# Kernel optimization log

Hardware: AMD Instinct MI355X
Metric: run time of the kernel (lower is better)

The kernel has to match this reference:

```python
import jax, jax.numpy as jnp
import numpy as np

D_MODEL, D_HIDDEN, N_EXPERTS = 1024, 4096, 8
CAP_FACTOR, LBL_COEF, ZLOSS_COEF = 1.25, 0.01, 0.0


def setup_inputs() -> dict:
    key = jax.random.key(0)
    ks = jax.random.split(key, 4)
    B, T = 4, 2048
    x = jax.random.normal(ks[0], (B, T, D_MODEL), dtype=jnp.float32)
    # router linear
    Wr = jax.random.normal(ks[1], (D_MODEL, N_EXPERTS), jnp.float32) / np.sqrt(D_MODEL).astype(np.float32)
    br = jnp.zeros((N_EXPERTS,), jnp.float32)
    # per-expert MLP: fc1 [D->H], gelu, fc2 [H->D]
    W1 = jax.random.normal(ks[2], (N_EXPERTS, D_MODEL, D_HIDDEN), jnp.float32) / np.sqrt(D_MODEL).astype(np.float32)
    b1 = jnp.zeros((N_EXPERTS, D_HIDDEN), jnp.float32)
    W2 = jax.random.normal(ks[3], (N_EXPERTS, D_HIDDEN, D_MODEL), jnp.float32) / np.sqrt(D_HIDDEN).astype(np.float32)
    b2 = jnp.zeros((N_EXPERTS, D_MODEL), jnp.float32)
    return {"x": x, "Wr": Wr, "br": br, "W1": W1, "b1": b1, "W2": W2, "b2": b2}


def reference(x, Wr, br, W1, b1, W2, b2):
    B, T, D = x.shape
    N = B * T
    E = Wr.shape[1]
    cap = int(CAP_FACTOR * (N / E) + 1)  # static Python int

    h = x.reshape(N, D)
    # --- Top1Router ---
    logits = h @ Wr + br                              # [N, E]
    probs = jax.nn.softmax(logits, axis=-1)
    top1 = jnp.argmax(probs, axis=-1)                 # [N]
    w = jnp.take_along_axis(probs, top1[:, None], axis=1)  # [N, 1]
    assign = jax.nn.one_hot(top1, E, dtype=jnp.float32)    # constant wrt grads
    importance = probs.mean(axis=0)
    load = jax.lax.stop_gradient(assign).mean(axis=0)
    lb_loss = E * jnp.sum(importance * load)
    z_loss = jnp.mean(jax.nn.logsumexp(logits, axis=-1) ** 2)

    # --- capacity-based dispatch (first `cap` tokens per expert, token order) ---
    pos = (jnp.cumsum(assign, axis=0) * assign).sum(axis=-1).astype(jnp.int32) - 1  # [N] slot within expert
    keep = pos < cap
    slot = jnp.where(keep, pos, cap)  # dropped tokens -> overflow slot `cap`
    xe = jnp.zeros((E, cap + 1, D), x.dtype).at[top1, slot].set(h)[:, :cap]  # [E, cap, D]

    # --- per-expert MLP as grouped GEMMs ---
    he = jax.nn.gelu(jnp.einsum('ecd,edh->ech', xe, W1) + b1[:, None, :])    # [E, cap, H]
    ye = jnp.einsum('ech,ehd->ecd', he, W2) + b2[:, None, :]                 # [E, cap, D]

    # --- combine (gather back, scale by router weight, zero dropped) ---
    out = ye[top1, jnp.minimum(pos, cap - 1)] * w   # [N, D]
    out = jnp.where(keep[:, None], out, jnp.zeros((), x.dtype))
    y = out.reshape(B, T, D)
    aux = LBL_COEF * lb_loss + ZLOSS_COEF * z_loss
    return (y, aux)
```

## Files before the change

### kernel.cpp

```cpp
#include <hip/hip_runtime.h>
#include <hip/hip_bf16.h>

#define N_TOK 8192
#define DM    1024
#define DH    4096
#define NE    8
#define CAP   1281
#define CAPR  1408
#define ISTR  1536

typedef unsigned short u16;
typedef __attribute__((ext_vector_type(8))) __bf16 bf16x8;
typedef __attribute__((ext_vector_type(8))) short short8;
typedef __attribute__((ext_vector_type(4))) float f4;

__device__ __forceinline__ u16 f2bf(float f){
  union { float f; unsigned u; } v; v.f = f;
  unsigned r = v.u + 0x7fffu + ((v.u >> 16) & 1u);
  return (u16)(r >> 16);
}

__device__ __forceinline__ float gelu_fast(float v){
  float u = 0.7978845608028654f * (v + 0.044715f * v * v * v);
  return v * __builtin_amdgcn_rcpf(1.0f + __expf(-2.0f * u));
}

__device__ __forceinline__ void gl2lds16(const void* g, void* l){
  __builtin_amdgcn_global_load_lds((const __attribute__((address_space(1))) void*)g,
                                   (__attribute__((address_space(3))) void*)l, 16, 0, 0);
}

__global__ __launch_bounds__(256) void cvt_x_k(const float* __restrict__ in, u16* __restrict__ out){
  int i = blockIdx.x * 256 + threadIdx.x;
  const f4* p = (const f4*)in + (size_t)i * 2;
  f4 a = p[0], b = p[1];
  short8 o;
  o[0]=(short)f2bf(a[0]); o[1]=(short)f2bf(a[1]); o[2]=(short)f2bf(a[2]); o[3]=(short)f2bf(a[3]);
  o[4]=(short)f2bf(b[0]); o[5]=(short)f2bf(b[1]); o[6]=(short)f2bf(b[2]); o[7]=(short)f2bf(b[3]);
  *(short8*)(out + (size_t)i*8) = o;
}

__global__ __launch_bounds__(256) void tcvt_k(const float* __restrict__ in, u16* __restrict__ out,
                                              int K, int Nn){
  __shared__ float tile[64][68];
  size_t mb = (size_t)blockIdx.z * (size_t)K * (size_t)Nn;
  const float* ip = in + mb;
  u16* op = out + mb;
  int n0 = blockIdx.x*64, k0 = blockIdx.y*64;
  int t = threadIdx.x;
  int kr = t>>4, nc = (t&15)*4;
  #pragma unroll
  for (int ii=0;ii<4;ii++){
    f4 v = *(const f4*)&ip[(size_t)(k0+kr+16*ii)*Nn + n0 + nc];
    tile[kr+16*ii][nc+0] = v[0]; tile[kr+16*ii][nc+1] = v[1];
    tile[kr+16*ii][nc+2] = v[2]; tile[kr+16*ii][nc+3] = v[3];
  }
  __syncthreads();
  int nr = t>>2, kc = (t&3)*16;
  short8 o0, o1;
  #pragma unroll
  for (int c=0;c<8;c++){
    o0[c] = (short)f2bf(tile[kc+c][nr]);
    o1[c] = (short)f2bf(tile[kc+8+c][nr]);
  }
  *(short8*)&op[(size_t)(n0+nr)*K + k0 + kc] = o0;
  *(short8*)&op[(size_t)(n0+nr)*K + k0 + kc + 8] = o1;
}

__global__ __launch_bounds__(256) void router_k(const float* __restrict__ x, const float* __restrict__ Wr,
    const float* __restrict__ br, int* __restrict__ top1, float* __restrict__ wgt,
    float* __restrict__ impSum){
  __shared__ float pSh[4][8];
  int wid = threadIdx.x >> 6, lane = threadIdx.x & 63;
  int n = blockIdx.x * 4 + wid;
  const float* xr = x + (size_t)n * DM;
  float acc[8];
  #pragma unroll
  for (int e=0;e<8;e++) acc[e]=0.f;
  #pragma unroll
  for (int c=0;c<4;c++){
    int d0 = c*256 + lane*4;
    f4 xv = *(const f4*)(xr + d0);
    #pragma unroll
    for (int j=0;j<4;j++){
      const float* wrow = Wr + (size_t)(d0+j)*NE;
      float xs = xv[j];
      #pragma unroll
      for (int e=0;e<8;e++) acc[e] = fmaf(xs, wrow[e], acc[e]);
    }
  }
  #pragma unroll
  for (int off=32; off>0; off>>=1){
    #pragma unroll
    for (int e=0;e<8;e++) acc[e] += __shfl_down(acc[e], off, 64);
  }
  if (lane==0){
    float lg[8]; float mx = -1e30f;
    #pragma unroll
    for (int e=0;e<8;e++){ lg[e] = acc[e] + br[e]; mx = fmaxf(mx, lg[e]); }
    float p[8], s=0.f;
    #pragma unroll
    for (int e=0;e<8;e++){ p[e] = expf(lg[e]-mx); s += p[e]; }
    int bt=0; float bv=lg[0];
    #pragma unroll
    for (int e=1;e<8;e++){ if (lg[e]>bv){ bv=lg[e]; bt=e; } }
    float inv = 1.f/s;
    top1[n] = bt; wgt[n] = p[bt]*inv;
    #pragma unroll
    for (int e=0;e<8;e++) pSh[wid][e] = p[e]*inv;
  }
  __syncthreads();
  if (threadIdx.x < 8){
    int e = threadIdx.x;
    atomicAdd(&impSum[e], pSh[0][e]+pSh[1][e]+pSh[2][e]+pSh[3][e]);
  }
}

__global__ __launch_bounds__(1024) void scan_k(const int* __restrict__ top1, int* __restrict__ idx,
    int* __restrict__ cnt, int* __restrict__ rawcnt, int* __restrict__ dropList,
    int* __restrict__ nDrop, const float* __restrict__ impSum, float* __restrict__ auxOut){
  __shared__ int waveCnt[16][8];
  __shared__ int wavePre[16][8];
  __shared__ int chunkTot[8];
  __shared__ int base_s[8];
  int tid = threadIdx.x, wid = tid>>6, lane = tid&63;
  if (tid < 8) base_s[tid] = 0;
  __syncthreads();
  for (int c=0;c<8;c++){
    int t = c*1024 + tid;
    int e = top1[t];
    int myPre = 0;
    #pragma unroll
    for (int ex=0; ex<8; ex++){
      unsigned long long mk = __ballot(e == ex);
      if (lane == 0) waveCnt[wid][ex] = __popcll(mk);
      if (ex == e) myPre = __popcll(mk & ((1ull<<lane)-1ull));
    }
    __syncthreads();
    if (tid < 8){
      int run = 0;
      for (int wv=0; wv<16; wv++){ wavePre[wv][tid] = run; run += waveCnt[wv][tid]; }
      chunkTot[tid] = run;
    }
    __syncthreads();
    int pos = base_s[e] + wavePre[wid][e] + myPre;
    if (pos < CAP) idx[e*ISTR + pos] = t;
    else { int d = atomicAdd(nDrop, 1); dropList[d] = t; }
    __syncthreads();
    if (tid < 8) base_s[tid] += chunkTot[tid];
    __syncthreads();
  }
  if (tid < 8){
    rawcnt[tid] = base_s[tid];
    cnt[tid] = base_s[tid] < CAP ? base_s[tid] : CAP;
  }
  if (tid == 0){
    float s = 0.f;
    for (int e=0;e<8;e++) s += (impSum[e]*(1.f/N_TOK)) * ((float)base_s[e]*(1.f/N_TOK));
    *auxOut = 0.01f * 8.f * s;
  }
}

__global__ __launch_bounds__(256) void zdrop_k(const int* __restrict__ dropList,
    const int* __restrict__ nDrop, float* __restrict__ y){
  int nd = *nDrop;
  for (int i = blockIdx.x; i < nd; i += gridDim.x){
    int t = dropList[i];
    f4* row = (f4*)(y + (size_t)t * DM);
    f4 z; z[0]=0.f; z[1]=0.f; z[2]=0.f; z[3]=0.f;
    row[threadIdx.x] = z;
  }
}

#define SA(buf, h, kt) do{ \
  gl2lds16(aS[(h)*2+0] + (size_t)(kt)*64, &lds[(buf)*16384 + ((h)*2+0)*4096 + t*8]); \
  gl2lds16(aS[(h)*2+1] + (size_t)(kt)*64, &lds[(buf)*16384 + ((h)*2+1)*4096 + t*8]); }while(0)
#define SBg(buf, h, kt) do{ \
  gl2lds16(bS[(h)*2+0] + (size_t)(kt)*64, &lds[32768 + (buf)*16384 + ((h)*2+0)*4096 + t*8]); \
  gl2lds16(bS[(h)*2+1] + (size_t)(kt)*64, &lds[32768 + (buf)*16384 + ((h)*2+1)*4096 + t*8]); }while(0)

#define LDA(buf, m, kk) (*(const bf16x8*)&lds[(buf)*16384 + (aBase ^ ((kk)*32)) + (m)*1024])
#define LDB(buf, n, kk) (*(const bf16x8*)&lds[32768 + (buf)*16384 + (bBase ^ ((kk)*32)) + (n)*1024])

#define PHASE(buf, q, STAGES, PREBAR) do{ \
  bf16x8 a_[2][2]; \
  if ((q)==0){ \
    _Pragma("unroll") for (int n_=0;n_<4;n_++) \
      _Pragma("unroll") for (int kk_=0;kk_<2;kk_++) Bf[n_][kk_] = LDB(buf, n_, kk_); \
  } \
  _Pragma("unroll") for (int j_=0;j_<2;j_++) \
    _Pragma("unroll") for (int kk_=0;kk_<2;kk_++) a_[j_][kk_] = LDA(buf, 2*(q)+j_, kk_); \
  STAGES; \
  __builtin_amdgcn_s_barrier(); \
  asm volatile("s_waitcnt lgkmcnt(0)" ::: "memory"); \
  __builtin_amdgcn_sched_barrier(0); \
  __builtin_amdgcn_s_setprio(1); \
  _Pragma("unroll") for (int j_=0;j_<2;j_++) \
    _Pragma("unroll") for (int n_=0;n_<4;n_++) \
      _Pragma("unroll") for (int kk_=0;kk_<2;kk_++) \
        acc[2*(q)+j_][n_] = __builtin_amdgcn_mfma_f32_16x16x32_bf16(a_[j_][kk_], Bf[n_][kk_], acc[2*(q)+j_][n_], 0,0,0); \
  __builtin_amdgcn_s_setprio(0); \
  PREBAR; \
  __builtin_amdgcn_s_barrier(); \
}while(0)

#define VMC4 asm volatile("s_waitcnt vmcnt(4)" ::: "memory")
#define NOP2 (void)0

__global__ __launch_bounds__(512, 2) void gemm1_k(
    const u16* __restrict__ Xb, const u16* __restrict__ W1T,
    const float* __restrict__ b1, const int* __restrict__ idx,
    const int* __restrict__ cnt, u16* __restrict__ He)
{
  int e = blockIdx.z, mt = blockIdx.y, nt = blockIdx.x;
  int cn = cnt[e];
  if (mt*256 >= cn) return;
  __shared__ __align__(16) u16 lds[65536];
  int t = threadIdx.x, lane = t&63, wid = t>>6;
  int waveM = wid>>2, waveN = wid&3;
  int rA = lane&15, kb = lane>>4, s = rA&7;

  const u16* aS[4]; const u16* bS[4];
  #pragma unroll
  for (int j=0;j<4;j++){
    int pos = j*512 + t;
    int row = pos>>3, ch = pos&7;
    int gcb = ch ^ (row&7);
    int slotrow = mt*256 + row;
    int token = (slotrow < cn) ? idx[e*ISTR + slotrow] : 0;
    aS[j] = Xb + (size_t)token*DM + gcb*8;
    bS[j] = W1T + ((size_t)e*DH + nt*256 + row)*DM + gcb*8;
  }
  f4 acc[8][4];
  #pragma unroll
  for (int m=0;m<8;m++)
    #pragma unroll
    for (int n=0;n<4;n++)
      #pragma unroll
      for (int j=0;j<4;j++) acc[m][n][j]=0.f;

  int aBase = (waveM*128 + rA)*64 + (kb ^ s)*8;
  int bBase = (waveN*64  + rA)*64 + (kb ^ s)*8;
  bf16x8 Bf[4][2];

  SBg(0,0,0); SBg(0,1,0); SA(0,0,0); SA(0,1,0); SBg(1,0,1); SBg(1,1,1);
  VMC4;
  __builtin_amdgcn_s_barrier();

  const int NT = DM/64;
  #pragma unroll 1
  for (int i=0;i<NT/2;i++){
    int kt1 = 2*i+1;
    int kt2 = (2*i+2 < NT) ? 2*i+2 : NT-1;
    int kt3 = (2*i+3 < NT) ? 2*i+3 : NT-1;
    PHASE(0,0, SA(1,0,kt1), NOP2);
    PHASE(0,1, { SA(1,1,kt1); SBg(0,0,kt2); }, NOP2);
    PHASE(0,2, SBg(0,1,kt2), NOP2);
    PHASE(0,3, NOP2, VMC4);
    PHASE(1,0, SA(0,0,kt2), NOP2);
    PHASE(1,1, { SA(0,1,kt2); SBg(1,0,kt3); }, NOP2);
    PHASE(1,2, SBg(1,1,kt3), NOP2);
    PHASE(1,3, NOP2, VMC4);
  }
  asm volatile("s_waitcnt vmcnt(0)" ::: "memory");

  int rG = lane>>4;
  #pragma unroll
  for (int n=0;n<4;n++){
    int col = nt*256 + waveN*64 + n*16 + rA;
    float bias = b1[e*DH + col];
    #pragma unroll
    for (int m=0;m<8;m++){
      int slot = mt*256 + waveM*128 + m*16 + rG*4;
      if (slot < CAPR){
        u16* dst = He + ((size_t)e*CAPR + slot)*DH + col;
        #pragma unroll
        for (int j=0;j<4;j++){
          float v = acc[m][n][j] + bias;
          dst[(size_t)j*DH] = f2bf(gelu_fast(v));
        }
      }
    }
  }
}

__global__ __launch_bounds__(512, 2) void gemm2_k(
    const u16* __restrict__ He, const u16* __restrict__ W2T,
    const float* __restrict__ b2, const int* __restrict__ idx,
    const int* __restrict__ cnt, const float* __restrict__ wgt,
    float* __restrict__ y)
{
  int e = blockIdx.z, mt = blockIdx.y, nt = blockIdx.x;
  int cn = cnt[e];
  if (mt*256 >= cn) return;
  __shared__ __align__(16) u16 lds[65536];
  int t = threadIdx.x, lane = t&63, wid = t>>6;
  int waveM = wid>>2, waveN = wid&3;
  int rA = lane&15, kb = lane>>4, s = rA&7;

  const u16* aS[4]; const u16* bS[4];
  #pragma unroll
  for (int j=0;j<4;j++){
    int pos = j*512 + t;
    int row = pos>>3, ch = pos&7;
    int gcb = ch ^ (row&7);
    int srow = mt*256 + row; if (srow >= cn) srow = cn-1;
    aS[j] = He  + ((size_t)e*CAPR + srow)*DH + gcb*8;
    bS[j] = W2T + ((size_t)e*DM + nt*256 + row)*DH + gcb*8;
  }
  f4 acc[8][4];
  #pragma unroll
  for (int m=0;m<8;m++)
    #pragma unroll
    for (int n=0;n<4;n++)
      #pragma unroll
      for (int j=0;j<4;j++) acc[m][n][j]=0.f;

  int aBase = (waveM*128 + rA)*64 + (kb ^ s)*8;
  int bBase = (waveN*64  + rA)*64 + (kb ^ s)*8;
  bf16x8 Bf[4][2];

  SBg(0,0,0); SBg(0,1,0); SA(0,0,0); SA(0,1,0); SBg(1,0,1); SBg(1,1,1);
  VMC4;
  __builtin_amdgcn_s_barrier();

  const int NT = DH/64;
  #pragma unroll 1
  for (int i=0;i<NT/2;i++){
    int kt1 = 2*i+1;
    int kt2 = (2*i+2 < NT) ? 2*i+2 : NT-1;
    int kt3 = (2*i+3 < NT) ? 2*i+3 : NT-1;
    PHASE(0,0, SA(1,0,kt1), NOP2);
    PHASE(0,1, { SA(1,1,kt1); SBg(0,0,kt2); }, NOP2);
    PHASE(0,2, SBg(0,1,kt2), NOP2);
    PHASE(0,3, NOP2, VMC4);
    PHASE(1,0, SA(0,0,kt2), NOP2);
    PHASE(1,1, { SA(0,1,kt2); SBg(1,0,kt3); }, NOP2);
    PHASE(1,2, SBg(1,1,kt3), NOP2);
    PHASE(1,3, NOP2, VMC4);
  }
  asm volatile("s_waitcnt vmcnt(0)" ::: "memory");

  int rG = lane>>4;
  float bias_[4];
  #pragma unroll
  for (int n=0;n<4;n++) bias_[n] = b2[e*DM + nt*256 + waveN*64 + n*16 + rA];
  #pragma unroll
  for (int m=0;m<8;m++){
    int slot0 = mt*256 + waveM*128 + m*16 + rG*4;
    #pragma unroll
    for (int j=0;j<4;j++){
      int slot = slot0 + j;
      bool valid = slot < cn;
      int tk = valid ? idx[e*ISTR + slot] : 0;
      float wv = valid ? wgt[tk] : 0.f;
      float* yr = y + (size_t)tk*DM;
      #pragma unroll
      for (int n=0;n<4;n++){
        int col = nt*256 + waveN*64 + n*16 + rA;
        if (valid) yr[col] = (acc[m][n][j] + bias_[n]) * wv;
      }
    }
  }
}

extern "C" void kernel_launch(void* const* d_in, const int* in_sizes, int n_in,
                              void* d_out, int out_size, void* d_ws, size_t ws_size,
                              hipStream_t stream){
  const float* x  = (const float*)d_in[0];
  const float* Wr = (const float*)d_in[1];
  const float* br = (const float*)d_in[2];
  const float* W1 = (const float*)d_in[3];
  const float* b1 = (const float*)d_in[4];
  const float* W2 = (const float*)d_in[5];
  const float* b2 = (const float*)d_in[6];
  float* y = (float*)d_out;

  char* ws = (char*)d_ws;
  u16* Xb  = (u16*)(ws);
  u16* W1T = (u16*)(ws + 16777216ull);
  u16* W2T = (u16*)(ws + 16777216ull + 67108864ull);
  u16* He  = (u16*)(ws + 16777216ull + 2ull*67108864ull);
  char* tail = ws + 16777216ull + 2ull*67108864ull + (size_t)NE*CAPR*DH*2ull;
  int*   top1 = (int*)(tail);
  float* wgt  = (float*)(tail + 32768);
  int*   idx  = (int*)(tail + 65536);
  int*   drop = (int*)(tail + 65536 + 49152);
  float* impSum = (float*)(tail + 65536 + 49152 + 32768);
  int*   nDrop  = (int*)((char*)impSum + 32);
  int*   cnt    = nDrop + 1;
  int*   rawcnt = cnt + 8;

  hipMemsetAsync(impSum, 0, 64, stream);

  cvt_x_k<<<4096, 256, 0, stream>>>(x, Xb);
  tcvt_k<<<dim3(64,16,8), 256, 0, stream>>>(W1, W1T, DM, DH);
  tcvt_k<<<dim3(16,64,8), 256, 0, stream>>>(W2, W2T, DH, DM);
  router_k<<<2048, 256, 0, stream>>>(x, Wr, br, top1, wgt, impSum);
  scan_k<<<1, 1024, 0, stream>>>(top1, idx, cnt, rawcnt, drop, nDrop, impSum,
                                 y + (size_t)N_TOK*DM);
  zdrop_k<<<64, 256, 0, stream>>>(drop, nDrop, y);
  gemm1_k<<<dim3(DH/256, 6, NE), 512, 0, stream>>>(Xb, W1T, b1, idx, cnt, He);
  gemm2_k<<<dim3(DM/256, 6, NE), 512, 0, stream>>>(He, W2T, b2, idx, cnt, wgt, y);

  (void)in_sizes; (void)n_in; (void)out_size; (void)ws_size;
}
```

Baseline: 376.1 us.

## Fuse x bf16 conversion into router and restructure GEMM k-tile pipeline

The standalone x-to-bf16 conversion kernel is removed, and the router now writes the bf16 copy while it already reads x. This saves one launch and one full pass over x. Both expert GEMMs also replace the eight-phase double-buffer schedule with a per-k-tile macro that waits on vmcnt(6) and issues A and B prefetches for the next tiles between the four MFMA sub-phases. The new schedule changes load ordering and barrier placement, so it risks races or less overlap if the wait counts are wrong.

```diff
diff --git a/kernel.cpp b/kernel.cpp
--- a/kernel.cpp
+++ b/kernel.cpp
@@ -12,6 +12,7 @@
 typedef unsigned short u16;
 typedef __attribute__((ext_vector_type(8))) __bf16 bf16x8;
 typedef __attribute__((ext_vector_type(8))) short short8;
+typedef __attribute__((ext_vector_type(4))) short s16x4;
 typedef __attribute__((ext_vector_type(4))) float f4;
 
 __device__ __forceinline__ u16 f2bf(float f){
@@ -28,16 +29,6 @@
 __device__ __forceinline__ void gl2lds16(const void* g, void* l){
   __builtin_amdgcn_global_load_lds((const __attribute__((address_space(1))) void*)g,
                                    (__attribute__((address_space(3))) void*)l, 16, 0, 0);
-}
-
-__global__ __launch_bounds__(256) void cvt_x_k(const float* __restrict__ in, u16* __restrict__ out){
-  int i = blockIdx.x * 256 + threadIdx.x;
-  const f4* p = (const f4*)in + (size_t)i * 2;
-  f4 a = p[0], b = p[1];
-  short8 o;
-  o[0]=(short)f2bf(a[0]); o[1]=(short)f2bf(a[1]); o[2]=(short)f2bf(a[2]); o[3]=(short)f2bf(a[3]);
-  o[4]=(short)f2bf(b[0]); o[5]=(short)f2bf(b[1]); o[6]=(short)f2bf(b[2]); o[7]=(short)f2bf(b[3]);
-  *(short8*)(out + (size_t)i*8) = o;
 }
 
 __global__ __launch_bounds__(256) void tcvt_k(const float* __restrict__ in, u16* __restrict__ out,
@@ -68,12 +59,13 @@
 }
 
 __global__ __launch_bounds__(256) void router_k(const float* __restrict__ x, const float* __restrict__ Wr,
-    const float* __restrict__ br, int* __restrict__ top1, float* __restrict__ wgt,
-    float* __restrict__ impSum){
+    const float* __restrict__ br, u16* __restrict__ Xb, int* __restrict__ top1,
+    float* __restrict__ wgt, float* __restrict__ impSum){
   __shared__ float pSh[4][8];
   int wid = threadIdx.x >> 6, lane = threadIdx.x & 63;
   int n = blockIdx.x * 4 + wid;
   const float* xr = x + (size_t)n * DM;
+  u16* xbr = Xb + (size_t)n * DM;
   float acc[8];
   #pragma unroll
   for (int e=0;e<8;e++) acc[e]=0.f;
@@ -81,6 +73,10 @@
   for (int c=0;c<4;c++){
     int d0 = c*256 + lane*4;
     f4 xv = *(const f4*)(xr + d0);
+    s16x4 xb;
+    #pragma unroll
+    for (int j=0;j<4;j++) xb[j] = (short)f2bf(xv[j]);
+    *(s16x4*)(xbr + d0) = xb;
     #pragma unroll
     for (int j=0;j<4;j++){
       const float* wrow = Wr + (size_t)(d0+j)*NE;
@@ -172,40 +168,63 @@
   }
 }
 
-#define SA(buf, h, kt) do{ \
-  gl2lds16(aS[(h)*2+0] + (size_t)(kt)*64, &lds[(buf)*16384 + ((h)*2+0)*4096 + t*8]); \
-  gl2lds16(aS[(h)*2+1] + (size_t)(kt)*64, &lds[(buf)*16384 + ((h)*2+1)*4096 + t*8]); }while(0)
-#define SBg(buf, h, kt) do{ \
-  gl2lds16(bS[(h)*2+0] + (size_t)(kt)*64, &lds[32768 + (buf)*16384 + ((h)*2+0)*4096 + t*8]); \
-  gl2lds16(bS[(h)*2+1] + (size_t)(kt)*64, &lds[32768 + (buf)*16384 + ((h)*2+1)*4096 + t*8]); }while(0)
 
 #define LDA(buf, m, kk) (*(const bf16x8*)&lds[(buf)*16384 + (aBase ^ ((kk)*32)) + (m)*1024])
 #define LDB(buf, n, kk) (*(const bf16x8*)&lds[32768 + (buf)*16384 + (bBase ^ ((kk)*32)) + (n)*1024])
 
-#define PHASE(buf, q, STAGES, PREBAR) do{ \
-  bf16x8 a_[2][2]; \
-  if ((q)==0){ \
-    _Pragma("unroll") for (int n_=0;n_<4;n_++) \
-      _Pragma("unroll") for (int kk_=0;kk_<2;kk_++) Bf[n_][kk_] = LDB(buf, n_, kk_); \
-  } \
-  _Pragma("unroll") for (int j_=0;j_<2;j_++) \
-    _Pragma("unroll") for (int kk_=0;kk_<2;kk_++) a_[j_][kk_] = LDA(buf, 2*(q)+j_, kk_); \
-  STAGES; \
-  __builtin_amdgcn_s_barrier(); \
-  asm volatile("s_waitcnt lgkmcnt(0)" ::: "memory"); \
-  __builtin_amdgcn_sched_barrier(0); \
-  __builtin_amdgcn_s_setprio(1); \
+#define SA_J(buf, j, kc) gl2lds16(aS[j] + (size_t)(kc)*64, &lds[(buf)*16384 + ((j)*512 + t)*8])
+#define SB_ALLM(buf, kc) do{ \
+  gl2lds16(bS[0] + (size_t)(kc)*64, &lds[32768 + (buf)*16384 + (0*512 + t)*8]); \
+  gl2lds16(bS[1] + (size_t)(kc)*64, &lds[32768 + (buf)*16384 + (1*512 + t)*8]); \
+  gl2lds16(bS[2] + (size_t)(kc)*64, &lds[32768 + (buf)*16384 + (2*512 + t)*8]); \
+  gl2lds16(bS[3] + (size_t)(kc)*64, &lds[32768 + (buf)*16384 + (3*512 + t)*8]); }while(0)
+
+#define LGKM0 do{ asm volatile("s_waitcnt lgkmcnt(0)" ::: "memory"); \
+                  __builtin_amdgcn_sched_barrier(0); }while(0)
+
+#define MFMA_PAIR(q) \
   _Pragma("unroll") for (int j_=0;j_<2;j_++) \
     _Pragma("unroll") for (int n_=0;n_<4;n_++) \
       _Pragma("unroll") for (int kk_=0;kk_<2;kk_++) \
-        acc[2*(q)+j_][n_] = __builtin_amdgcn_mfma_f32_16x16x32_bf16(a_[j_][kk_], Bf[n_][kk_], acc[2*(q)+j_][n_], 0,0,0); \
-  __builtin_amdgcn_s_setprio(0); \
-  PREBAR; \
+        acc[2*(q)+j_][n_] = __builtin_amdgcn_mfma_f32_16x16x32_bf16(a_[j_][kk_], Bf[n_][kk_], acc[2*(q)+j_][n_], 0,0,0);
+
+#define KTILE(buf, ktv, NTv) do{ \
+  int kc1 = (ktv)+1 < (NTv) ? (ktv)+1 : (NTv)-1; \
+  int kc2 = (ktv)+2 < (NTv) ? (ktv)+2 : (NTv)-1; \
+  bf16x8 a_[2][2]; \
+   \
+  asm volatile("s_waitcnt vmcnt(6)" ::: "memory"); \
   __builtin_amdgcn_s_barrier(); \
+  _Pragma("unroll") for (int n_=0;n_<4;n_++){ Bf[n_][0] = LDB(buf,n_,0); Bf[n_][1] = LDB(buf,n_,1); } \
+  a_[0][0]=LDA(buf,0,0); a_[0][1]=LDA(buf,0,1); a_[1][0]=LDA(buf,1,0); a_[1][1]=LDA(buf,1,1); \
+  SA_J((buf)^1, 1, kc1); SA_J((buf)^1, 3, kc1); \
+  LGKM0; \
+  __builtin_amdgcn_s_setprio(1); MFMA_PAIR(0); __builtin_amdgcn_s_setprio(0); \
+   \
+  __builtin_amdgcn_s_barrier(); \
+  a_[0][0]=LDA(buf,2,0); a_[0][1]=LDA(buf,2,1); a_[1][0]=LDA(buf,3,0); a_[1][1]=LDA(buf,3,1); \
+  SB_ALLM(buf, kc2); \
+  LGKM0; \
+  __builtin_amdgcn_s_setprio(1); MFMA_PAIR(1); __builtin_amdgcn_s_setprio(0); \
+   \
+  __builtin_amdgcn_s_barrier(); \
+  a_[0][0]=LDA(buf,4,0); a_[0][1]=LDA(buf,4,1); a_[1][0]=LDA(buf,5,0); a_[1][1]=LDA(buf,5,1); \
+  SA_J(buf, 0, kc2); SA_J(buf, 2, kc2); \
+  LGKM0; \
+  __builtin_amdgcn_s_setprio(1); MFMA_PAIR(2); __builtin_amdgcn_s_setprio(0); \
+   \
+  __builtin_amdgcn_s_barrier(); \
+  a_[0][0]=LDA(buf,6,0); a_[0][1]=LDA(buf,6,1); a_[1][0]=LDA(buf,7,0); a_[1][1]=LDA(buf,7,1); \
+  LGKM0; \
+  __builtin_amdgcn_s_setprio(1); MFMA_PAIR(3); __builtin_amdgcn_s_setprio(0); \
 }while(0)
 
-#define VMC4 asm volatile("s_waitcnt vmcnt(4)" ::: "memory")
-#define NOP2 (void)0
+#define GEMM_PROLOGUE() do{ \
+  SB_ALLM(0, 0); \
+  SA_J(0,0,0); SA_J(0,2,0); \
+  SA_J(0,1,0); SA_J(0,3,0); \
+  SB_ALLM(1, 1); \
+  SA_J(1,0,1); SA_J(1,2,1); }while(0)
 
 __global__ __launch_bounds__(512, 2) void gemm1_k(
     const u16* __restrict__ Xb, const u16* __restrict__ W1T,
@@ -243,26 +262,14 @@
   int bBase = (waveN*64  + rA)*64 + (kb ^ s)*8;
   bf16x8 Bf[4][2];
 
-  SBg(0,0,0); SBg(0,1,0); SA(0,0,0); SA(0,1,0); SBg(1,0,1); SBg(1,1,1);
-  VMC4;
-  __builtin_amdgcn_s_barrier();
-
+  GEMM_PROLOGUE();
   const int NT = DM/64;
   #pragma unroll 1
   for (int i=0;i<NT/2;i++){
-    int kt1 = 2*i+1;
-    int kt2 = (2*i+2 < NT) ? 2*i+2 : NT-1;
-    int kt3 = (2*i+3 < NT) ? 2*i+3 : NT-1;
-    PHASE(0,0, SA(1,0,kt1), NOP2);
-    PHASE(0,1, { SA(1,1,kt1); SBg(0,0,kt2); }, NOP2);
-    PHASE(0,2, SBg(0,1,kt2), NOP2);
-    PHASE(0,3, NOP2, VMC4);
-    PHASE(1,0, SA(0,0,kt2), NOP2);
-    PHASE(1,1, { SA(0,1,kt2); SBg(1,0,kt3); }, NOP2);
-    PHASE(1,2, SBg(1,1,kt3), NOP2);
-    PHASE(1,3, NOP2, VMC4);
-  }
-  asm volatile("s_waitcnt vmcnt(0)" ::: "memory");
+    KTILE(0, 2*i,   NT);
+    KTILE(1, 2*i+1, NT);
+  }
+  asm volatile("s_waitcnt vmcnt(0) lgkmcnt(0)" ::: "memory");
 
   int rG = lane>>4;
   #pragma unroll
@@ -320,26 +327,14 @@
   int bBase = (waveN*64  + rA)*64 + (kb ^ s)*8;
   bf16x8 Bf[4][2];
 
-  SBg(0,0,0); SBg(0,1,0); SA(0,0,0); SA(0,1,0); SBg(1,0,1); SBg(1,1,1);
-  VMC4;
-  __builtin_amdgcn_s_barrier();
-
+  GEMM_PROLOGUE();
   const int NT = DH/64;
   #pragma unroll 1
   for (int i=0;i<NT/2;i++){
-    int kt1 = 2*i+1;
-    int kt2 = (2*i+2 < NT) ? 2*i+2 : NT-1;
-    int kt3 = (2*i+3 < NT) ? 2*i+3 : NT-1;
-    PHASE(0,0, SA(1,0,kt1), NOP2);
-    PHASE(0,1, { SA(1,1,kt1); SBg(0,0,kt2); }, NOP2);
-    PHASE(0,2, SBg(0,1,kt2), NOP2);
-    PHASE(0,3, NOP2, VMC4);
-    PHASE(1,0, SA(0,0,kt2), NOP2);
-    PHASE(1,1, { SA(0,1,kt2); SBg(1,0,kt3); }, NOP2);
-    PHASE(1,2, SBg(1,1,kt3), NOP2);
-    PHASE(1,3, NOP2, VMC4);
-  }
-  asm volatile("s_waitcnt vmcnt(0)" ::: "memory");
+    KTILE(0, 2*i,   NT);
+    KTILE(1, 2*i+1, NT);
+  }
+  asm volatile("s_waitcnt vmcnt(0) lgkmcnt(0)" ::: "memory");
 
   int rG = lane>>4;
   float bias_[4];
@@ -391,12 +386,11 @@
   int*   cnt    = nDrop + 1;
   int*   rawcnt = cnt + 8;
 
-  hipMemsetAsync(impSum, 0, 64, stream);
-
-  cvt_x_k<<<4096, 256, 0, stream>>>(x, Xb);
+  (void)hipMemsetAsync(impSum, 0, 64, stream);
+
   tcvt_k<<<dim3(64,16,8), 256, 0, stream>>>(W1, W1T, DM, DH);
   tcvt_k<<<dim3(16,64,8), 256, 0, stream>>>(W2, W2T, DH, DM);
-  router_k<<<2048, 256, 0, stream>>>(x, Wr, br, top1, wgt, impSum);
+  router_k<<<2048, 256, 0, stream>>>(x, Wr, br, Xb, top1, wgt, impSum);
   scan_k<<<1, 1024, 0, stream>>>(top1, idx, cnt, rawcnt, drop, nDrop, impSum,
                                  y + (size_t)N_TOK*DM);
   zdrop_k<<<64, 256, 0, stream>>>(drop, nDrop, y);
```

After: 356.2 us. -5.3%, faster.
